# Optimization experiments

Measured on AMD Instinct MI355X. Metric: run time of the kernel, lower is better.

## Reference

```python
import jax, jax.numpy as jnp
import numpy as np

B = 16384
F = 1024
DELTA = 0.3
LAMB = 0.0005


def setup_inputs() -> dict:
    key = jax.random.key(0)
    k1, k2, k3, k4 = jax.random.split(key, 4)
    skt = jax.random.normal(k1, (B, F), dtype=jnp.float32)
    imgp = jax.random.normal(k2, (B, F), dtype=jnp.float32)
    imgn = jax.random.normal(k3, (B, F), dtype=jnp.float32)
    eye = jnp.eye(F, dtype=jnp.float32)
    w = eye + 0.05 * jax.random.normal(k4, (F, F), dtype=jnp.float32)
    return {"skt": skt, "imgp": imgp, "imgn": imgn, "w": w, "eye": eye}


def _distance(v1, v2, w, w_rowsum, w_colsum):
    # sum_{i,j} w[i,j] * (v1[:,i] - v2[:,j])**2
    #   = (v1**2) @ w.sum(1) - 2 * v1 @ w @ v2^T (diag) + (v2**2) @ w.sum(0)
    cross = ((v1 @ w) * v2).sum(axis=-1)  # [B]
    return (v1 * v1) @ w_rowsum - 2.0 * cross + (v2 * v2) @ w_colsum


def reference(skt, imgp, imgn, w, eye):
    w_rowsum = w.sum(axis=1)  # [F]
    w_colsum = w.sum(axis=0)  # [F]
    dp = _distance(skt, imgp, w, w_rowsum, w_colsum)  # [B]
    dn = _distance(skt, imgn, w, w_rowsum, w_colsum)  # [B]
    hinge = jnp.maximum(DELTA + dp - dn, 0.0).mean()
    dw = w - eye
    regu = jnp.abs(dw).sum() + jnp.sqrt((dw * dw).sum())
    return hinge + LAMB * regu
```

## Files before the change

### kernel.cpp

```cpp
#include <hip/hip_runtime.h>
#include <hip/hip_bf16.h>

#define FDIM 1024
#define BROWS 16384
#define DELTA_C 0.3f
#define LAMB_C 0.0005f

typedef __bf16 bf8v __attribute__((ext_vector_type(8)));
typedef float f4v __attribute__((ext_vector_type(4)));
typedef unsigned short u16;
typedef u16 u16x8 __attribute__((ext_vector_type(8)));

#define WS_PABS_OFF 4160
#define WS_PSQ_OFF 4672
#define WS_ROWACC_OFF 8192
#define WS_WB_OFF 131072
#define WS_SKTB_OFF (131072 + (1u << 21))
#define WS_NEED_FULL ((size_t)WS_SKTB_OFF + ((size_t)1 << 25))

__device__ __forceinline__ u16 f2bf(float f) {
  unsigned u = __builtin_bit_cast(unsigned, f);
  u += 0x7fffu + ((u >> 16) & 1u);
  return (u16)(u >> 16);
}

__device__ __forceinline__ void gload_lds16(const void* g, void* l) {
  __builtin_amdgcn_global_load_lds(
      (const __attribute__((address_space(1))) unsigned int*)g,
      (__attribute__((address_space(3))) unsigned int*)l, 16, 0, 0);
}

template <bool DO_A>
__global__ __launch_bounds__(256) void prep_all(const float* __restrict__ w,
                                                const float* __restrict__ skt,
                                                float* __restrict__ colsum,
                                                float* __restrict__ pabs,
                                                float* __restrict__ psq,
                                                u16* __restrict__ wb,
                                                u16* __restrict__ sktb) {
  __shared__ char smem_u[17440];
  const int t = threadIdx.x;
  const int bid = blockIdx.x;

  if (bid < 128) {
    u16(*tile)[1024] = (u16(*)[1024])smem_u;
    float* red = (float*)(smem_u + 16384);
    const int b = bid;
    const int k0 = b * 8;
    const int col = t * 4;

    float cs0 = 0.f, cs1 = 0.f, cs2 = 0.f, cs3 = 0.f;
    float aacc = 0.f, sacc = 0.f;
#pragma unroll
    for (int i = 0; i < 8; ++i) {
      const int gk = k0 + i;
      const float4 v = *(const float4*)(w + (size_t)gk * FDIM + col);
      ushort4 bb;
      bb.x = f2bf(v.x); bb.y = f2bf(v.y); bb.z = f2bf(v.z); bb.w = f2bf(v.w);
      *(ushort4*)(&tile[i][col]) = bb;
      cs0 += v.x; cs1 += v.y; cs2 += v.z; cs3 += v.w;
      const float d0 = v.x - (gk == col + 0 ? 1.f : 0.f);
      const float d1 = v.y - (gk == col + 1 ? 1.f : 0.f);
      const float d2 = v.z - (gk == col + 2 ? 1.f : 0.f);
      const float d3 = v.w - (gk == col + 3 ? 1.f : 0.f);
      aacc += fabsf(d0) + fabsf(d1) + fabsf(d2) + fabsf(d3);
      sacc += d0 * d0 + d1 * d1 + d2 * d2 + d3 * d3;
    }
    atomicAdd(&colsum[col + 0], cs0);
    atomicAdd(&colsum[col + 1], cs1);
    atomicAdd(&colsum[col + 2], cs2);
    atomicAdd(&colsum[col + 3], cs3);
#pragma unroll
    for (int off = 1; off < 64; off <<= 1) {
      aacc += __shfl_xor(aacc, off);
      sacc += __shfl_xor(sacc, off);
    }
    const int wv = t >> 6;
    if ((t & 63) == 0) { red[wv] = aacc; red[4 + wv] = sacc; }
    __syncthreads();
    if (t == 0) pabs[b] = red[0] + red[1] + red[2] + red[3];
    if (t == 1) psq[b] = red[4] + red[5] + red[6] + red[7];
#pragma unroll
    for (int j = 0; j < 4; ++j) {
      const int n = col + j;
      u16x8 pk;
#pragma unroll
      for (int e = 0; e < 8; ++e) pk[e] = tile[e][n];
      *(u16x8*)(wb + ((size_t)b * FDIM + n) * 8) = pk;
    }
  } else if constexpr (DO_A) {
    u16(*tile)[136] = (u16(*)[136])smem_u;
    const int ab = bid - 128;
    const int mb = ab >> 3;
    const int kb = ab & 7;
    const int m0 = mb * 64, k0 = kb * 128;
#pragma unroll
    for (int i = 0; i < 8; ++i) {
      const int fid = i * 256 + t;
      const int ml = fid >> 5;
      const int c4 = fid & 31;
      const float4 v = *(const float4*)(skt + (size_t)(m0 + ml) * FDIM + k0 + c4 * 4);
      ushort4 b;
      b.x = f2bf(v.x); b.y = f2bf(v.y); b.z = f2bf(v.z); b.w = f2bf(v.w);
      *(ushort4*)(&tile[ml][c4 * 4]) = b;
    }
    __syncthreads();
    const int ks0 = k0 >> 3;
#pragma unroll
    for (int i = 0; i < 4; ++i) {
      const int uid = i * 256 + t;
      const int si = uid >> 6;
      const int ml = uid & 63;
      const u16x8 pk = *(const u16x8*)(&tile[ml][si * 8]);
      *(u16x8*)(sktb + ((size_t)(ks0 + si) * BROWS + m0 + ml) * 8) = pk;
    }
  }
}

template <bool PRE>
__global__ __launch_bounds__(512, 4) void hofel_main(
    const float* __restrict__ skt, const float* __restrict__ imgp,
    const float* __restrict__ imgn, const u16* __restrict__ wb,
    const u16* __restrict__ sktb, const float* __restrict__ colsum,
    float* __restrict__ rowacc) {
  __shared__ u16 ldsT[2][12288];
  __shared__ float lds_cs[128];

  const int t = threadIdx.x;
  const int lane = t & 63;
  const int wid = t >> 6;
  const int l15 = lane & 15;
  const int l4 = lane >> 4;

  const int swz = (blockIdx.x & 7) * 64 + (blockIdx.x >> 3);
  const int mt = swz >> 3, nt = swz & 7;
  const int m0 = mt * 256, n0 = nt * 128;

  const int wr = wid >> 1, wc = wid & 1;
  const int wm = wr * 64, wn = wc * 64;

  f4v acc[4][4];
#pragma unroll
  for (int mi = 0; mi < 4; ++mi)
#pragma unroll
    for (int ni = 0; ni < 4; ++ni) {
      f4v z = {0.f, 0.f, 0.f, 0.f};
      acc[mi][ni] = z;
    }

  auto stage = [&](int buf, int kt) {
    if constexpr (PRE) {
#pragma unroll
      for (int r = 0; r < 3; ++r) {
        const int o = r * 8192 + wid * 1024;
        const int ol = o + lane * 16;
        const char* src;
        if (ol < 16384) {
          const int s = ol >> 12;
          const int m = (ol >> 4) & 255;
          src = (const char*)(sktb + ((size_t)(kt * 4 + s) * BROWS + m0 + m) * 8);
        } else {
          const int o2 = ol - 16384;
          const int s = o2 >> 11;
          const int n = (o2 >> 4) & 127;
          src = (const char*)(wb + ((size_t)(kt * 4 + s) * FDIM + n0 + n) * 8);
        }
        gload_lds16(src, (char*)ldsT[buf] + o);
      }
    } else {
      {
        const int o = wid * 1024;
        const int ol = o + lane * 16;
        const int s = ol >> 11;
        const int n = (ol >> 4) & 127;
        gload_lds16((const char*)(wb + ((size_t)(kt * 4 + s) * FDIM + n0 + n) * 8),
                    (char*)ldsT[buf] + 16384 + o);
      }
      const int m = t >> 1, h = t & 1;
      const float* ap = skt + (size_t)(m0 + m) * FDIM + kt * 32 + h * 16;
#pragma unroll
      for (int q = 0; q < 2; ++q) {
        const float4 v0 = *(const float4*)(ap + q * 8);
        const float4 v1 = *(const float4*)(ap + q * 8 + 4);
        u16x8 pk;
        pk[0] = f2bf(v0.x); pk[1] = f2bf(v0.y); pk[2] = f2bf(v0.z); pk[3] = f2bf(v0.w);
        pk[4] = f2bf(v1.x); pk[5] = f2bf(v1.y); pk[6] = f2bf(v1.z); pk[7] = f2bf(v1.w);
        *(u16x8*)((char*)ldsT[buf] + (h * 2 + q) * 4096 + m * 16) = pk;
      }
    }
  };

  stage(0, 0);
  if (t < 128) lds_cs[t] = colsum[n0 + t];
  __syncthreads();

  int cur = 0;
  for (int kt = 0; kt < 32; ++kt) {
    if (kt < 31) stage(cur ^ 1, kt + 1);

    const char* bufb = (const char*)ldsT[cur];
    bf8v aF[4], bF[4];
#pragma unroll
    for (int mi = 0; mi < 4; ++mi)
      aF[mi] = *(const bf8v*)(bufb + l4 * 4096 + (wm + mi * 16 + l15) * 16);
#pragma unroll
    for (int ni = 0; ni < 4; ++ni)
      bF[ni] = *(const bf8v*)(bufb + 16384 + l4 * 2048 + (wn + ni * 16 + l15) * 16);
#pragma unroll
    for (int mi = 0; mi < 4; ++mi)
#pragma unroll
      for (int ni = 0; ni < 4; ++ni)
        acc[mi][ni] = __builtin_amdgcn_mfma_f32_16x16x32_bf16(aF[mi], bF[ni], acc[mi][ni], 0, 0, 0);

    __syncthreads();
    cur ^= 1;
  }

  {
    float(*eT)[68] = (float(*)[68])((char*)ldsT + wid * 4352);
    const int r = l15;
    const int qb = l4;
#pragma unroll
    for (int mi = 0; mi < 4; ++mi) {
#pragma unroll
      for (int ni = 0; ni < 4; ++ni)
#pragma unroll
        for (int rr = 0; rr < 4; ++rr)
          eT[l4 * 4 + rr][ni * 16 + l15] = acc[mi][ni][rr];
      const int rowg = m0 + wm + mi * 16 + r;
      const float* pr = imgp + (size_t)rowg * FDIM + n0 + wn;
      const float* nr = imgn + (size_t)rowg * FDIM + n0 + wn;
      float part = 0.f;
#pragma unroll
      for (int i = 0; i < 4; ++i) {
        const int q = qb + 4 * i;
        const f4v T = *(const f4v*)&eT[r][q * 4];
        const float4 p = *(const float4*)(pr + q * 4);
        const float4 n = *(const float4*)(nr + q * 4);
        const f4v cs = *(const f4v*)&lds_cs[wn + q * 4];
        part += (p.x - n.x) * (-2.f * T[0] + (p.x + n.x) * cs[0]);
        part += (p.y - n.y) * (-2.f * T[1] + (p.y + n.y) * cs[1]);
        part += (p.z - n.z) * (-2.f * T[2] + (p.z + n.z) * cs[2]);
        part += (p.w - n.w) * (-2.f * T[3] + (p.w + n.w) * cs[3]);
      }
      part += __shfl_xor(part, 16);
      part += __shfl_xor(part, 32);
      if (lane < 16) atomicAdd(rowacc + rowg, part);
      __syncthreads();
    }
  }
}

__global__ __launch_bounds__(1024) void hinge_reduce(const float* __restrict__ rowacc,
                                                     float* __restrict__ wsf) {
  __shared__ float part[16];
  const int t = threadIdx.x;
  const int id = blockIdx.x * 1024 + t;
  float v = fmaxf(DELTA_C + rowacc[id], 0.f);
#pragma unroll
  for (int off = 1; off < 64; off <<= 1) v += __shfl_xor(v, off);
  if ((t & 63) == 0) part[t >> 6] = v;
  __syncthreads();
  if (t < 16) {
    float x = part[t];
#pragma unroll
    for (int off = 1; off < 16; off <<= 1) x += __shfl_xor(x, off);
    if (t == 0) atomicAdd(&wsf[0], x);
  }
}

__global__ __launch_bounds__(128) void finalize_k(const float* __restrict__ wsf,
                                                  const float* __restrict__ pabs,
                                                  const float* __restrict__ psq,
                                                  float* __restrict__ out) {
  __shared__ float ra[2], rs[2];
  const int t = threadIdx.x;
  float a = pabs[t], s = psq[t];
#pragma unroll
  for (int off = 1; off < 64; off <<= 1) {
    a += __shfl_xor(a, off);
    s += __shfl_xor(s, off);
  }
  if ((t & 63) == 0) { ra[t >> 6] = a; rs[t >> 6] = s; }
  __syncthreads();
  if (t == 0)
    out[0] = wsf[0] * (1.f / (float)BROWS) +
             LAMB_C * ((ra[0] + ra[1]) + sqrtf(rs[0] + rs[1]));
}

extern "C" void kernel_launch(void* const* d_in, const int* in_sizes, int n_in,
                              void* d_out, int out_size, void* d_ws, size_t ws_size,
                              hipStream_t stream) {
  const float* skt  = (const float*)d_in[0];
  const float* imgp = (const float*)d_in[1];
  const float* imgn = (const float*)d_in[2];
  const float* w    = (const float*)d_in[3];

  float* wsf = (float*)d_ws;
  float* colsum = wsf + 16;
  float* pabs = (float*)((char*)d_ws + WS_PABS_OFF);
  float* psq = (float*)((char*)d_ws + WS_PSQ_OFF);
  float* rowacc = (float*)((char*)d_ws + WS_ROWACC_OFF);
  u16* wb = (u16*)((char*)d_ws + WS_WB_OFF);
  u16* sktb = (u16*)((char*)d_ws + WS_SKTB_OFF);
  float* out = (float*)d_out;

  hipMemsetAsync(d_ws, 0, WS_ROWACC_OFF + BROWS * sizeof(float), stream);

  if (ws_size >= WS_NEED_FULL) {
    prep_all<true><<<128 + 2048, 256, 0, stream>>>(w, skt, colsum, pabs, psq, wb, sktb);
    hofel_main<true><<<512, 512, 0, stream>>>(skt, imgp, imgn, wb, sktb, colsum, rowacc);
  } else {
    prep_all<false><<<128, 256, 0, stream>>>(w, skt, colsum, pabs, psq, wb, sktb);
    hofel_main<false><<<512, 512, 0, stream>>>(skt, imgp, imgn, wb, sktb, colsum, rowacc);
  }

  hinge_reduce<<<16, 1024, 0, stream>>>(rowacc, wsf);
  finalize_k<<<1, 128, 0, stream>>>(wsf, pabs, psq, out);
}
```

Measured before the change: 87.06 us.

## Switch main GEMM to FP8 MFMA with FP8-packed operand staging

The prep kernel now converts skt and w to FP8 (e4m3) in a k-packed layout instead of bf16, and the main kernel uses the 16x16x128 scaled FP8 MFMA with a 128x128 tile, 256 threads and 8 k-steps. This halves the bytes of the pre-converted operands and cuts the number of matrix instructions per output. The cost is much lower precision in the cross term, which could push the loss outside tolerance, plus a new dynamic-LDS tile shape and occupancy. A non-pipelined bf16 fallback kernel handles the small-workspace case.

```diff
diff --git a/kernel.cpp b/kernel.cpp
--- a/kernel.cpp
+++ b/kernel.cpp
@@ -8,15 +8,18 @@
 
 typedef __bf16 bf8v __attribute__((ext_vector_type(8)));
 typedef float f4v __attribute__((ext_vector_type(4)));
+typedef int i8v __attribute__((ext_vector_type(8)));
 typedef unsigned short u16;
 typedef u16 u16x8 __attribute__((ext_vector_type(8)));
 
 #define WS_PABS_OFF 4160
 #define WS_PSQ_OFF 4672
 #define WS_ROWACC_OFF 8192
-#define WS_WB_OFF 131072
-#define WS_SKTB_OFF (131072 + (1u << 21))
-#define WS_NEED_FULL ((size_t)WS_SKTB_OFF + ((size_t)1 << 25))
+#define WS_WB8_OFF 131072
+#define WS_SKTB8_OFF (131072 + (1u << 20))
+#define WS_NEED ((size_t)WS_SKTB8_OFF + ((size_t)1 << 24))
+
+#define SMEM_MAIN (65536 + 512)
 
 __device__ __forceinline__ u16 f2bf(float f) {
   unsigned u = __builtin_bit_cast(unsigned, f);
@@ -30,24 +33,23 @@
       (__attribute__((address_space(3))) unsigned int*)l, 16, 0, 0);
 }
 
-template <bool DO_A>
+template <bool FULL>
 __global__ __launch_bounds__(256) void prep_all(const float* __restrict__ w,
                                                 const float* __restrict__ skt,
                                                 float* __restrict__ colsum,
                                                 float* __restrict__ pabs,
                                                 float* __restrict__ psq,
-                                                u16* __restrict__ wb,
-                                                u16* __restrict__ sktb) {
-  __shared__ char smem_u[17440];
+                                                char* __restrict__ wb8,
+                                                char* __restrict__ sktb8) {
+  __shared__ float red[8];
   const int t = threadIdx.x;
   const int bid = blockIdx.x;
 
   if (bid < 128) {
-    u16(*tile)[1024] = (u16(*)[1024])smem_u;
-    float* red = (float*)(smem_u + 16384);
     const int b = bid;
     const int k0 = b * 8;
     const int col = t * 4;
+    float wv[8][4];
 
     float cs0 = 0.f, cs1 = 0.f, cs2 = 0.f, cs3 = 0.f;
     float aacc = 0.f, sacc = 0.f;
@@ -55,9 +57,7 @@
     for (int i = 0; i < 8; ++i) {
       const int gk = k0 + i;
       const float4 v = *(const float4*)(w + (size_t)gk * FDIM + col);
-      ushort4 bb;
-      bb.x = f2bf(v.x); bb.y = f2bf(v.y); bb.z = f2bf(v.z); bb.w = f2bf(v.w);
-      *(ushort4*)(&tile[i][col]) = bb;
+      wv[i][0] = v.x; wv[i][1] = v.y; wv[i][2] = v.z; wv[i][3] = v.w;
       cs0 += v.x; cs1 += v.y; cs2 += v.z; cs3 += v.w;
       const float d0 = v.x - (gk == col + 0 ? 1.f : 0.f);
       const float d1 = v.y - (gk == col + 1 ? 1.f : 0.f);
@@ -75,56 +75,53 @@
       aacc += __shfl_xor(aacc, off);
       sacc += __shfl_xor(sacc, off);
     }
-    const int wv = t >> 6;
-    if ((t & 63) == 0) { red[wv] = aacc; red[4 + wv] = sacc; }
+    const int wv_ = t >> 6;
+    if ((t & 63) == 0) { red[wv_] = aacc; red[4 + wv_] = sacc; }
     __syncthreads();
     if (t == 0) pabs[b] = red[0] + red[1] + red[2] + red[3];
     if (t == 1) psq[b] = red[4] + red[5] + red[6] + red[7];
-#pragma unroll
-    for (int j = 0; j < 4; ++j) {
-      const int n = col + j;
-      u16x8 pk;
-#pragma unroll
-      for (int e = 0; e < 8; ++e) pk[e] = tile[e][n];
-      *(u16x8*)(wb + ((size_t)b * FDIM + n) * 8) = pk;
-    }
-  } else if constexpr (DO_A) {
-    u16(*tile)[136] = (u16(*)[136])smem_u;
+    if constexpr (FULL) {
+#pragma unroll
+      for (int j = 0; j < 4; ++j) {
+        int lo = __builtin_amdgcn_cvt_pk_fp8_f32(wv[0][j], wv[1][j], 0, false);
+        lo = __builtin_amdgcn_cvt_pk_fp8_f32(wv[2][j], wv[3][j], lo, true);
+        int hi = __builtin_amdgcn_cvt_pk_fp8_f32(wv[4][j], wv[5][j], 0, false);
+        hi = __builtin_amdgcn_cvt_pk_fp8_f32(wv[6][j], wv[7][j], hi, true);
+        int2 pk; pk.x = lo; pk.y = hi;
+        *(int2*)(wb8 + ((size_t)(b >> 2) * 1024 + col + j) * 32 + (b & 3) * 8) = pk;
+      }
+    }
+  } else if constexpr (FULL) {
     const int ab = bid - 128;
-    const int mb = ab >> 3;
-    const int kb = ab & 7;
-    const int m0 = mb * 64, k0 = kb * 128;
-#pragma unroll
-    for (int i = 0; i < 8; ++i) {
-      const int fid = i * 256 + t;
-      const int ml = fid >> 5;
-      const int c4 = fid & 31;
-      const float4 v = *(const float4*)(skt + (size_t)(m0 + ml) * FDIM + k0 + c4 * 4);
-      ushort4 b;
-      b.x = f2bf(v.x); b.y = f2bf(v.y); b.z = f2bf(v.z); b.w = f2bf(v.w);
-      *(ushort4*)(&tile[ml][c4 * 4]) = b;
-    }
-    __syncthreads();
-    const int ks0 = k0 >> 3;
-#pragma unroll
-    for (int i = 0; i < 4; ++i) {
-      const int uid = i * 256 + t;
-      const int si = uid >> 6;
-      const int ml = uid & 63;
-      const u16x8 pk = *(const u16x8*)(&tile[ml][si * 8]);
-      *(u16x8*)(sktb + ((size_t)(ks0 + si) * BROWS + m0 + ml) * 8) = pk;
-    }
-  }
-}
-
-template <bool PRE>
-__global__ __launch_bounds__(512, 4) void hofel_main(
-    const float* __restrict__ skt, const float* __restrict__ imgp,
-    const float* __restrict__ imgn, const u16* __restrict__ wb,
-    const u16* __restrict__ sktb, const float* __restrict__ colsum,
-    float* __restrict__ rowacc) {
-  __shared__ u16 ldsT[2][12288];
-  __shared__ float lds_cs[128];
+    const int mb = ab >> 3, kb = ab & 7;
+    const int m0 = mb * 64, k0 = kb * 128, kg0 = kb * 4;
+    const int m = t & 63, kg = t >> 6;
+    const float* sp = skt + (size_t)(m0 + m) * FDIM + k0 + kg * 32;
+    int wds[8];
+#pragma unroll
+    for (int q = 0; q < 4; ++q) {
+      const float4 a = *(const float4*)(sp + q * 8);
+      const float4 b = *(const float4*)(sp + q * 8 + 4);
+      int w0 = __builtin_amdgcn_cvt_pk_fp8_f32(a.x, a.y, 0, false);
+      w0 = __builtin_amdgcn_cvt_pk_fp8_f32(a.z, a.w, w0, true);
+      int w1 = __builtin_amdgcn_cvt_pk_fp8_f32(b.x, b.y, 0, false);
+      w1 = __builtin_amdgcn_cvt_pk_fp8_f32(b.z, b.w, w1, true);
+      wds[2 * q] = w0; wds[2 * q + 1] = w1;
+    }
+    char* dst = sktb8 + ((size_t)(kg0 + kg) * BROWS + m0 + m) * 32;
+    int4 lo; lo.x = wds[0]; lo.y = wds[1]; lo.z = wds[2]; lo.w = wds[3];
+    int4 hi; hi.x = wds[4]; hi.y = wds[5]; hi.z = wds[6]; hi.w = wds[7];
+    *(int4*)dst = lo;
+    *(int4*)(dst + 16) = hi;
+  }
+}
+
+__global__ __launch_bounds__(256, 2) void hofel_main_fp8(
+    const float* __restrict__ imgp, const float* __restrict__ imgn,
+    const char* __restrict__ wb8, const char* __restrict__ sktb8,
+    const float* __restrict__ colsum, float* __restrict__ rowacc) {
+  extern __shared__ char smem[];
+  float* lds_cs = (float*)(smem + 65536);
 
   const int t = threadIdx.x;
   const int lane = t & 63;
@@ -132,12 +129,11 @@
   const int l15 = lane & 15;
   const int l4 = lane >> 4;
 
-  const int swz = (blockIdx.x & 7) * 64 + (blockIdx.x >> 3);
-  const int mt = swz >> 3, nt = swz & 7;
-  const int m0 = mt * 256, n0 = nt * 128;
-
-  const int wr = wid >> 1, wc = wid & 1;
-  const int wm = wr * 64, wn = wc * 64;
+  const int swz = (blockIdx.x & 7) * 128 + (blockIdx.x >> 3);
+  const int mt = swz >> 3, ntw = swz & 7;
+  const int m0 = mt * 128, n0 = ntw * 128;
+
+  const int wm = (wid >> 1) * 64, wn = (wid & 1) * 64;
 
   f4v acc[4][4];
 #pragma unroll
@@ -149,44 +145,21 @@
     }
 
   auto stage = [&](int buf, int kt) {
-    if constexpr (PRE) {
-#pragma unroll
-      for (int r = 0; r < 3; ++r) {
-        const int o = r * 8192 + wid * 1024;
-        const int ol = o + lane * 16;
-        const char* src;
-        if (ol < 16384) {
-          const int s = ol >> 12;
-          const int m = (ol >> 4) & 255;
-          src = (const char*)(sktb + ((size_t)(kt * 4 + s) * BROWS + m0 + m) * 8);
-        } else {
-          const int o2 = ol - 16384;
-          const int s = o2 >> 11;
-          const int n = (o2 >> 4) & 127;
-          src = (const char*)(wb + ((size_t)(kt * 4 + s) * FDIM + n0 + n) * 8);
-        }
-        gload_lds16(src, (char*)ldsT[buf] + o);
+    char* base = smem + buf * 32768;
+#pragma unroll
+    for (int r = 0; r < 8; ++r) {
+      const int o = r * 4096 + wid * 1024;
+      const int ol = o + lane * 16;
+      const char* src;
+      if (ol < 16384) {
+        const int kg = ol >> 12, ch = (ol >> 11) & 1, m = (ol >> 4) & 127;
+        src = sktb8 + ((size_t)(kt * 4 + kg) * BROWS + m0 + m) * 32 + ch * 16;
+      } else {
+        const int o2 = ol - 16384;
+        const int kg = o2 >> 12, ch = (o2 >> 11) & 1, n = (o2 >> 4) & 127;
+        src = wb8 + ((size_t)(kt * 4 + kg) * FDIM + n0 + n) * 32 + ch * 16;
       }
-    } else {
-      {
-        const int o = wid * 1024;
-        const int ol = o + lane * 16;
-        const int s = ol >> 11;
-        const int n = (ol >> 4) & 127;
-        gload_lds16((const char*)(wb + ((size_t)(kt * 4 + s) * FDIM + n0 + n) * 8),
-                    (char*)ldsT[buf] + 16384 + o);
-      }
-      const int m = t >> 1, h = t & 1;
-      const float* ap = skt + (size_t)(m0 + m) * FDIM + kt * 32 + h * 16;
-#pragma unroll
-      for (int q = 0; q < 2; ++q) {
-        const float4 v0 = *(const float4*)(ap + q * 8);
-        const float4 v1 = *(const float4*)(ap + q * 8 + 4);
-        u16x8 pk;
-        pk[0] = f2bf(v0.x); pk[1] = f2bf(v0.y); pk[2] = f2bf(v0.z); pk[3] = f2bf(v0.w);
-        pk[4] = f2bf(v1.x); pk[5] = f2bf(v1.y); pk[6] = f2bf(v1.z); pk[7] = f2bf(v1.w);
-        *(u16x8*)((char*)ldsT[buf] + (h * 2 + q) * 4096 + m * 16) = pk;
-      }
+      gload_lds16(src, base + o);
     }
   };
 
@@ -195,31 +168,42 @@
   __syncthreads();
 
   int cur = 0;
-  for (int kt = 0; kt < 32; ++kt) {
-    if (kt < 31) stage(cur ^ 1, kt + 1);
-
-    const char* bufb = (const char*)ldsT[cur];
-    bf8v aF[4], bF[4];
+  for (int kt = 0; kt < 8; ++kt) {
+    if (kt < 7) stage(cur ^ 1, kt + 1);
+
+    const char* bA = smem + cur * 32768;
+    const char* bB = bA + 16384;
+    i8v aF[4], bF[4];
+#pragma unroll
+    for (int mi = 0; mi < 4; ++mi) {
+      const int row = wm + mi * 16 + l15;
+      const int4 lo = *(const int4*)(bA + l4 * 4096 + row * 16);
+      const int4 hi = *(const int4*)(bA + l4 * 4096 + 2048 + row * 16);
+      i8v v = {lo.x, lo.y, lo.z, lo.w, hi.x, hi.y, hi.z, hi.w};
+      aF[mi] = v;
+    }
+#pragma unroll
+    for (int ni = 0; ni < 4; ++ni) {
+      const int row = wn + ni * 16 + l15;
+      const int4 lo = *(const int4*)(bB + l4 * 4096 + row * 16);
+      const int4 hi = *(const int4*)(bB + l4 * 4096 + 2048 + row * 16);
+      i8v v = {lo.x, lo.y, lo.z, lo.w, hi.x, hi.y, hi.z, hi.w};
+      bF[ni] = v;
+    }
 #pragma unroll
     for (int mi = 0; mi < 4; ++mi)
-      aF[mi] = *(const bf8v*)(bufb + l4 * 4096 + (wm + mi * 16 + l15) * 16);
-#pragma unroll
-    for (int ni = 0; ni < 4; ++ni)
-      bF[ni] = *(const bf8v*)(bufb + 16384 + l4 * 2048 + (wn + ni * 16 + l15) * 16);
-#pragma unroll
-    for (int mi = 0; mi < 4; ++mi)
 #pragma unroll
       for (int ni = 0; ni < 4; ++ni)
-        acc[mi][ni] = __builtin_amdgcn_mfma_f32_16x16x32_bf16(aF[mi], bF[ni], acc[mi][ni], 0, 0, 0);
+        acc[mi][ni] = __builtin_amdgcn_mfma_scale_f32_16x16x128_f8f6f4(
+            aF[mi], bF[ni], acc[mi][ni], 0, 0, 0, 0x7F7F7F7F, 0, 0x7F7F7F7F);
 
     __syncthreads();
     cur ^= 1;
   }
 
   {
-    float(*eT)[68] = (float(*)[68])((char*)ldsT + wid * 4352);
-    const int r = l15;
-    const int qb = l4;
+    float(*eT)[68] = (float(*)[68])(smem + wid * 4352);
+    const int r = l15, qb = l4;
 #pragma unroll
     for (int mi = 0; mi < 4; ++mi) {
 #pragma unroll
@@ -251,6 +235,101 @@
   }
 }
 
+__global__ __launch_bounds__(512, 4) void hofel_fb(
+    const float* __restrict__ skt, const float* __restrict__ imgp,
+    const float* __restrict__ imgn, const float* __restrict__ w,
+    const float* __restrict__ colsum, float* __restrict__ rowacc) {
+  __shared__ u16 ldsT[12288];
+  __shared__ float lds_cs[128];
+  const int t = threadIdx.x, lane = t & 63, wid = t >> 6;
+  const int l15 = lane & 15, l4 = lane >> 4;
+  const int swz = (blockIdx.x & 7) * 64 + (blockIdx.x >> 3);
+  const int mt = swz >> 3, nt = swz & 7;
+  const int m0 = mt * 256, n0 = nt * 128;
+  const int wm = (wid >> 1) * 64, wn = (wid & 1) * 64;
+
+  if (t < 128) lds_cs[t] = colsum[n0 + t];
+  f4v acc[4][4];
+#pragma unroll
+  for (int mi = 0; mi < 4; ++mi)
+#pragma unroll
+    for (int ni = 0; ni < 4; ++ni) {
+      f4v z = {0.f, 0.f, 0.f, 0.f};
+      acc[mi][ni] = z;
+    }
+
+  for (int kt = 0; kt < 32; ++kt) {
+    __syncthreads();
+    {
+      const int kc = t >> 2, s = t & 3;
+      u16x8 pk;
+#pragma unroll
+      for (int e = 0; e < 8; ++e)
+        pk[e] = f2bf(w[(size_t)(kt * 32 + s * 8 + e) * FDIM + n0 + kc]);
+      *(u16x8*)((char*)ldsT + 16384 + (s * 128 + kc) * 16) = pk;
+    }
+    {
+      const int m = t >> 1, h = t & 1;
+      const float* ap = skt + (size_t)(m0 + m) * FDIM + kt * 32 + h * 16;
+#pragma unroll
+      for (int q = 0; q < 2; ++q) {
+        const float4 v0 = *(const float4*)(ap + q * 8);
+        const float4 v1 = *(const float4*)(ap + q * 8 + 4);
+        u16x8 pk;
+        pk[0] = f2bf(v0.x); pk[1] = f2bf(v0.y); pk[2] = f2bf(v0.z); pk[3] = f2bf(v0.w);
+        pk[4] = f2bf(v1.x); pk[5] = f2bf(v1.y); pk[6] = f2bf(v1.z); pk[7] = f2bf(v1.w);
+        *(u16x8*)((char*)ldsT + (h * 2 + q) * 4096 + m * 16) = pk;
+      }
+    }
+    __syncthreads();
+    bf8v aF[4], bF[4];
+#pragma unroll
+    for (int mi = 0; mi < 4; ++mi)
+      aF[mi] = *(const bf8v*)((char*)ldsT + l4 * 4096 + (wm + mi * 16 + l15) * 16);
+#pragma unroll
+    for (int ni = 0; ni < 4; ++ni)
+      bF[ni] = *(const bf8v*)((char*)ldsT + 16384 + l4 * 2048 + (wn + ni * 16 + l15) * 16);
+#pragma unroll
+    for (int mi = 0; mi < 4; ++mi)
+#pragma unroll
+      for (int ni = 0; ni < 4; ++ni)
+        acc[mi][ni] = __builtin_amdgcn_mfma_f32_16x16x32_bf16(aF[mi], bF[ni], acc[mi][ni], 0, 0, 0);
+  }
+  __syncthreads();
+  {
+    float(*eT)[68] = (float(*)[68])((char*)ldsT + wid * 4352);
+    const int r = l15, qb = l4;
+#pragma unroll
+    for (int mi = 0; mi < 4; ++mi) {
+#pragma unroll
+      for (int ni = 0; ni < 4; ++ni)
+#pragma unroll
+        for (int rr = 0; rr < 4; ++rr)
+          eT[l4 * 4 + rr][ni * 16 + l15] = acc[mi][ni][rr];
+      const int rowg = m0 + wm + mi * 16 + r;
+      const float* pr = imgp + (size_t)rowg * FDIM + n0 + wn;
+      const float* nr = imgn + (size_t)rowg * FDIM + n0 + wn;
+      float part = 0.f;
+#pragma unroll
+      for (int i = 0; i < 4; ++i) {
+        const int q = qb + 4 * i;
+        const f4v T = *(const f4v*)&eT[r][q * 4];
+        const float4 p = *(const float4*)(pr + q * 4);
+        const float4 n = *(const float4*)(nr + q * 4);
+        const f4v cs = *(const f4v*)&lds_cs[wn + q * 4];
+        part += (p.x - n.x) * (-2.f * T[0] + (p.x + n.x) * cs[0]);
+        part += (p.y - n.y) * (-2.f * T[1] + (p.y + n.y) * cs[1]);
+        part += (p.z - n.z) * (-2.f * T[2] + (p.z + n.z) * cs[2]);
+        part += (p.w - n.w) * (-2.f * T[3] + (p.w + n.w) * cs[3]);
+      }
+      part += __shfl_xor(part, 16);
+      part += __shfl_xor(part, 32);
+      if (lane < 16) atomicAdd(rowacc + rowg, part);
+      __syncthreads();
+    }
+  }
+}
+
 __global__ __launch_bounds__(1024) void hinge_reduce(const float* __restrict__ rowacc,
                                                      float* __restrict__ wsf) {
   __shared__ float part[16];
@@ -301,18 +380,20 @@
   float* pabs = (float*)((char*)d_ws + WS_PABS_OFF);
   float* psq = (float*)((char*)d_ws + WS_PSQ_OFF);
   float* rowacc = (float*)((char*)d_ws + WS_ROWACC_OFF);
-  u16* wb = (u16*)((char*)d_ws + WS_WB_OFF);
-  u16* sktb = (u16*)((char*)d_ws + WS_SKTB_OFF);
+  char* wb8 = (char*)d_ws + WS_WB8_OFF;
+  char* sktb8 = (char*)d_ws + WS_SKTB8_OFF;
   float* out = (float*)d_out;
 
   hipMemsetAsync(d_ws, 0, WS_ROWACC_OFF + BROWS * sizeof(float), stream);
 
-  if (ws_size >= WS_NEED_FULL) {
-    prep_all<true><<<128 + 2048, 256, 0, stream>>>(w, skt, colsum, pabs, psq, wb, sktb);
-    hofel_main<true><<<512, 512, 0, stream>>>(skt, imgp, imgn, wb, sktb, colsum, rowacc);
+  if (ws_size >= WS_NEED) {
+    prep_all<true><<<128 + 2048, 256, 0, stream>>>(w, skt, colsum, pabs, psq, wb8, sktb8);
+    (void)hipFuncSetAttribute(reinterpret_cast<const void*>(hofel_main_fp8),
+                              hipFuncAttributeMaxDynamicSharedMemorySize, SMEM_MAIN);
+    hofel_main_fp8<<<1024, 256, SMEM_MAIN, stream>>>(imgp, imgn, wb8, sktb8, colsum, rowacc);
   } else {
-    prep_all<false><<<128, 256, 0, stream>>>(w, skt, colsum, pabs, psq, wb, sktb);
-    hofel_main<false><<<512, 512, 0, stream>>>(skt, imgp, imgn, wb, sktb, colsum, rowacc);
+    prep_all<false><<<128, 256, 0, stream>>>(w, skt, colsum, pabs, psq, wb8, sktb8);
+    hofel_fb<<<512, 512, 0, stream>>>(skt, imgp, imgn, w, colsum, rowacc);
   }
 
   hinge_reduce<<<16, 1024, 0, stream>>>(rowacc, wsf);
```

Result: faster. 76.00 us (-12.7%).
